# Kernel optimization log

Measured on AMD Instinct MI355X. Metric: run time of the kernel, lower is better.

Reference implementation:

```python
import jax, jax.numpy as jnp
import numpy as np

EYE_PENALTY = 1.0e6


def setup_inputs() -> dict:
    key = jax.random.key(0)
    k1, k2 = jax.random.split(key)
    B, NIN, NK, DK = 512, 1024, 128, 5
    x = jax.random.normal(k1, (B, NIN), dtype=jnp.float32)
    theta = jax.random.normal(k2, (NIN, NK, DK), dtype=jnp.float32) * 0.05
    log_weight_scale = jnp.zeros((NK, DK), dtype=jnp.float32)
    bias = jnp.full((NK,), -1.0, dtype=jnp.float32)
    return {"x": x, "theta": theta, "log_weight_scale": log_weight_scale, "bias": bias}


def reference(x, theta, log_weight_scale, bias):
    # kernel = theta * exp(log_weight_scale) / ||theta||_2 (norm over input dim)
    l2 = jnp.sqrt(jnp.sum(theta * theta, axis=0))            # [K, D]
    kernel = theta * (jnp.exp(log_weight_scale) / l2)[None]   # [NIN, K, D]
    actv = jnp.einsum('bi,ikd->bkd', x, kernel)               # [B, K, D]
    B = x.shape[0]
    # all-pairs L1 distance per kernel: [B, K, B]
    diff = actv[:, :, :, None] - jnp.transpose(actv, (1, 2, 0))[None]  # [B,K,D,B]
    abs_dif = jnp.sum(jnp.abs(diff), axis=2)                  # [B, K, B]
    abs_dif = abs_dif + EYE_PENALTY * jnp.eye(B, dtype=x.dtype)[:, None, :]
    f = jnp.sum(jnp.exp(-abs_dif), axis=2) + bias[None, :]    # [B, K]
    return jnp.concatenate([x, f], axis=1)                    # [B, NIN + K]
```

## Files before the change

### kernel.cpp

```cpp
#include <hip/hip_runtime.h>
#include <hip/hip_fp16.h>
#include <math.h>

constexpr int B    = 512;
constexpr int NIN  = 1024;
constexpr int NK   = 128;
constexpr int DK   = 5;
constexpr int NF   = NK * DK;
constexpr int NOUT = NIN + NK;
constexpr int SPLITK = 4;
constexpr int LDA = 88;
#define LOG2E 1.44269504088896f

typedef _Float16 f16x2 __attribute__((ext_vector_type(2)));
typedef _Float16 f16x4 __attribute__((ext_vector_type(4)));
typedef _Float16 f16x8 __attribute__((ext_vector_type(8)));
typedef float    f32x4 __attribute__((ext_vector_type(4)));

union H2 { __half2 h; f16x2 v; unsigned u; };

__global__ __launch_bounds__(256) void gemm_kernel(
        const float* __restrict__ x,
        const float* __restrict__ theta,
        float* __restrict__ actvP,
        float* __restrict__ ps) {
    __shared__ _Float16 Ath[64 * LDA];
    __shared__ _Float16 Bxh[64 * LDA];
    __shared__ float    red2[16][64];

    const int t    = threadIdx.x;
    const int tile = blockIdx.x >> 2;
    const int z    = blockIdx.x & 3;
    const int n0   = (tile >> 3) * 64;
    const int b0   = (tile & 7) * 64;
    const bool do_ps = (tile & 7) == 0;

    const int w   = t >> 6;
    const int l   = t & 63;
    const int r16 = l & 15;
    const int kg  = l >> 4;
    const int tk4 = t >> 4;
    const int tn4 = (t & 15) * 4;

    f32x4 acc0 = {0.f,0.f,0.f,0.f}, acc1 = {0.f,0.f,0.f,0.f};
    f32x4 acc2 = {0.f,0.f,0.f,0.f}, acc3 = {0.f,0.f,0.f,0.f};
    float sq0 = 0.f, sq1 = 0.f, sq2 = 0.f, sq3 = 0.f;

    for (int step = 0; step < 4; ++step) {
        const int kw = z * 256 + step * 64;
        const float4 v0 = *(const float4*)&theta[(kw + tk4*4 + 0)*NF + n0 + tn4];
        const float4 v1 = *(const float4*)&theta[(kw + tk4*4 + 1)*NF + n0 + tn4];
        const float4 v2 = *(const float4*)&theta[(kw + tk4*4 + 2)*NF + n0 + tn4];
        const float4 v3 = *(const float4*)&theta[(kw + tk4*4 + 3)*NF + n0 + tn4];
        if (do_ps) {
            sq0 += v0.x*v0.x + v1.x*v1.x + v2.x*v2.x + v3.x*v3.x;
            sq1 += v0.y*v0.y + v1.y*v1.y + v2.y*v2.y + v3.y*v3.y;
            sq2 += v0.z*v0.z + v1.z*v1.z + v2.z*v2.z + v3.z*v3.z;
            sq3 += v0.w*v0.w + v1.w*v1.w + v2.w*v2.w + v3.w*v3.w;
        }
        {
            f16x4 h;
            h[0]=(_Float16)v0.x; h[1]=(_Float16)v1.x; h[2]=(_Float16)v2.x; h[3]=(_Float16)v3.x;
            *(f16x4*)&Ath[(tn4+0)*LDA + tk4*4] = h;
            h[0]=(_Float16)v0.y; h[1]=(_Float16)v1.y; h[2]=(_Float16)v2.y; h[3]=(_Float16)v3.y;
            *(f16x4*)&Ath[(tn4+1)*LDA + tk4*4] = h;
            h[0]=(_Float16)v0.z; h[1]=(_Float16)v1.z; h[2]=(_Float16)v2.z; h[3]=(_Float16)v3.z;
            *(f16x4*)&Ath[(tn4+2)*LDA + tk4*4] = h;
            h[0]=(_Float16)v0.w; h[1]=(_Float16)v1.w; h[2]=(_Float16)v2.w; h[3]=(_Float16)v3.w;
            *(f16x4*)&Ath[(tn4+3)*LDA + tk4*4] = h;
        }
        #pragma unroll
        for (int i = 0; i < 4; ++i) {
            const int row = i * 16 + tk4;
            const float4 xv = *(const float4*)&x[(b0 + row)*NIN + kw + tn4];
            f16x4 h;
            h[0]=(_Float16)xv.x; h[1]=(_Float16)xv.y;
            h[2]=(_Float16)xv.z; h[3]=(_Float16)xv.w;
            *(f16x4*)&Bxh[row*LDA + tn4] = h;
        }
        __syncthreads();
        #pragma unroll
        for (int half = 0; half < 2; ++half) {
            const f16x8 av  = *(const f16x8*)&Ath[(w*16 + r16)*LDA + kg*8 + half*32];
            const f16x8 bv0 = *(const f16x8*)&Bxh[( 0 + r16)*LDA + kg*8 + half*32];
            const f16x8 bv1 = *(const f16x8*)&Bxh[(16 + r16)*LDA + kg*8 + half*32];
            const f16x8 bv2 = *(const f16x8*)&Bxh[(32 + r16)*LDA + kg*8 + half*32];
            const f16x8 bv3 = *(const f16x8*)&Bxh[(48 + r16)*LDA + kg*8 + half*32];
            acc0 = __builtin_amdgcn_mfma_f32_16x16x32_f16(av, bv0, acc0, 0, 0, 0);
            acc1 = __builtin_amdgcn_mfma_f32_16x16x32_f16(av, bv1, acc1, 0, 0, 0);
            acc2 = __builtin_amdgcn_mfma_f32_16x16x32_f16(av, bv2, acc2, 0, 0, 0);
            acc3 = __builtin_amdgcn_mfma_f32_16x16x32_f16(av, bv3, acc3, 0, 0, 0);
        }
        __syncthreads();
    }
    {
        float* dst = actvP + (size_t)z * NF * B
                   + (size_t)(n0 + w*16 + kg*4) * B + b0 + r16;
        #pragma unroll
        for (int j = 0; j < 4; ++j) {
            dst[j*B +  0] = acc0[j];
            dst[j*B + 16] = acc1[j];
            dst[j*B + 32] = acc2[j];
            dst[j*B + 48] = acc3[j];
        }
    }
    if (do_ps) {
        red2[tk4][tn4+0] = sq0; red2[tk4][tn4+1] = sq1;
        red2[tk4][tn4+2] = sq2; red2[tk4][tn4+3] = sq3;
        __syncthreads();
        if (t < 64) {
            float tot = 0.f;
            #pragma unroll
            for (int rr = 0; rr < 16; ++rr) tot += red2[rr][t];
            ps[z * NF + n0 + t] = tot;
        }
    }
}

__global__ __launch_bounds__(256) void rs_kernel(
        const float* __restrict__ actvP,
        const float* __restrict__ ps,
        const float* __restrict__ lws,
        __half* __restrict__ actv16) {
    const int t   = threadIdx.x;
    const int row = blockIdx.x * 2 + (t >> 7);
    const int c4  = (t & 127) * 4;

    const float nrm = ps[0*NF + row] + ps[1*NF + row]
                    + ps[2*NF + row] + ps[3*NF + row];
    const float s = __expf(lws[row]) * rsqrtf(nrm) * LOG2E;

    const float* p = actvP + (size_t)row * B + c4;
    float4 v0 = *(const float4*)(p + 0ull * NF * B);
    float4 v1 = *(const float4*)(p + 1ull * NF * B);
    float4 v2 = *(const float4*)(p + 2ull * NF * B);
    float4 v3 = *(const float4*)(p + 3ull * NF * B);
    f16x4 h;
    h[0] = (_Float16)((v0.x + v1.x + v2.x + v3.x) * s);
    h[1] = (_Float16)((v0.y + v1.y + v2.y + v3.y) * s);
    h[2] = (_Float16)((v0.z + v1.z + v2.z + v3.z) * s);
    h[3] = (_Float16)((v0.w + v1.w + v2.w + v3.w) * s);
    *(f16x4*)&actv16[(size_t)row * B + c4] = h;
}

__global__ __launch_bounds__(256) void pairwise_kernel(
        const __half* __restrict__ actv16,
        const float* __restrict__ bias,
        const float* __restrict__ x,
        float* __restrict__ out) {
    __shared__ __half a16s[DK * B];
    __shared__ float  red[8 * 64];

    const int k = blockIdx.x;
    const int e = blockIdx.y;
    const int t = threadIdx.x;

    if (e < 4) {
        const int row = k * 4 + e;
        ((float4*)out)[row * (NOUT/4) + t] = ((const float4*)x)[row * (NIN/4) + t];
    }

    {
        const uint4* src = (const uint4*)(actv16 + (size_t)k * DK * B);
        ((uint4*)a16s)[t] = src[t];
        if (t < 64) ((uint4*)a16s)[256 + t] = src[256 + t];
    }
    __syncthreads();

    const int g  = t >> 5;
    const int r  = t & 31;
    const int ba = e * 64 + r;
    const int bb = ba + 32;

    __half2 A2[DK], B2[DK];
    #pragma unroll
    for (int d = 0; d < DK; ++d) {
        A2[d] = __half2half2(a16s[d * B + ba]);
        B2[d] = __half2half2(a16s[d * B + bb]);
    }
    const H2 ones = {__half2half2(__float2half(1.0f))};

    float accA = 0.f, accB = 0.f;
    const int bp0 = g * 64;

    union W8 { f16x8 v; __half2 h[4]; };
    #pragma unroll 2
    for (int m = 0; m < 8; ++m) {
        const int bp = bp0 + m * 8;
        W8 w0, w1, w2, w3, w4;
        w0.v = *(const f16x8*)&a16s[0*B + bp];
        w1.v = *(const f16x8*)&a16s[1*B + bp];
        w2.v = *(const f16x8*)&a16s[2*B + bp];
        w3.v = *(const f16x8*)&a16s[3*B + bp];
        w4.v = *(const f16x8*)&a16s[4*B + bp];
        #pragma unroll
        for (int c = 0; c < 4; ++c) {
            __half2 dA = __habs2(__hsub2(A2[0], w0.h[c]));
            dA = __hadd2(dA, __habs2(__hsub2(A2[1], w1.h[c])));
            dA = __hadd2(dA, __habs2(__hsub2(A2[2], w2.h[c])));
            dA = __hadd2(dA, __habs2(__hsub2(A2[3], w3.h[c])));
            dA = __hadd2(dA, __habs2(__hsub2(A2[4], w4.h[c])));
            H2 eA; eA.h = h2exp2(__hneg2(dA));
            __half2 dB = __habs2(__hsub2(B2[0], w0.h[c]));
            dB = __hadd2(dB, __habs2(__hsub2(B2[1], w1.h[c])));
            dB = __hadd2(dB, __habs2(__hsub2(B2[2], w2.h[c])));
            dB = __hadd2(dB, __habs2(__hsub2(B2[3], w3.h[c])));
            dB = __hadd2(dB, __habs2(__hsub2(B2[4], w4.h[c])));
            H2 eB; eB.h = h2exp2(__hneg2(dB));
#if __has_builtin(__builtin_amdgcn_fdot2)
            accA = __builtin_amdgcn_fdot2(eA.v, ones.v, accA, false);
            accB = __builtin_amdgcn_fdot2(eB.v, ones.v, accB, false);
#else
            accA += __low2float(eA.h) + __high2float(eA.h);
            accB += __low2float(eB.h) + __high2float(eB.h);
#endif
        }
    }
    red[g * 64 + r]      = accA;
    red[g * 64 + 32 + r] = accB;
    __syncthreads();
    if (t < 64) {
        float f = -1.0f + bias[k];
        #pragma unroll
        for (int gg = 0; gg < 8; ++gg) f += red[gg * 64 + t];
        out[(e * 64 + t) * NOUT + NIN + k] = f;
    }
}

extern "C" void kernel_launch(void* const* d_in, const int* in_sizes, int n_in,
                              void* d_out, int out_size, void* d_ws, size_t ws_size,
                              hipStream_t stream) {
    const float* x     = (const float*)d_in[0];
    const float* theta = (const float*)d_in[1];
    const float* lws   = (const float*)d_in[2];
    const float* bias  = (const float*)d_in[3];
    float* out = (float*)d_out;

    char* wsb = (char*)d_ws;
    float*  ps     = (float*)wsb;
    float*  actvP  = (float*)(wsb + (64 << 10));
    __half* actv16 = (__half*)(wsb + (64 << 10) + 4 * sizeof(float) * NF * B);

    gemm_kernel<<<dim3(320), 256, 0, stream>>>(x, theta, actvP, ps);
    rs_kernel<<<dim3(320), 256, 0, stream>>>(actvP, ps, lws, actv16);
    pairwise_kernel<<<dim3(NK, 8), 256, 0, stream>>>(actv16, bias, x, out);
}
```

Before: 27.11 us.

## Raise GEMM split-K to 8 and load each K-chunk in a single pass

Doubles the split-K factor so the GEMM launches 640 blocks, each handling a 128-wide K slice loaded entirely into LDS at once. This removes the inner step loop and its per-step barriers, and issues all global loads up front for more memory-level parallelism. In exchange the split-K partial buffer doubles, so the reduction kernel reads twice as many partials. Register and LDS use per block also grow.

```diff
diff --git a/kernel.cpp b/kernel.cpp
--- a/kernel.cpp
+++ b/kernel.cpp
@@ -8,8 +8,8 @@
 constexpr int DK   = 5;
 constexpr int NF   = NK * DK;
 constexpr int NOUT = NIN + NK;
-constexpr int SPLITK = 4;
-constexpr int LDA = 88;
+constexpr int SPLITK = 8;
+constexpr int LDA = 136;
 #define LOG2E 1.44269504088896f
 
 typedef _Float16 f16x2 __attribute__((ext_vector_type(2)));
@@ -29,70 +29,82 @@
     __shared__ float    red2[16][64];
 
     const int t    = threadIdx.x;
-    const int tile = blockIdx.x >> 2;
-    const int z    = blockIdx.x & 3;
+    const int tile = blockIdx.x >> 3;
+    const int z    = blockIdx.x & 7;
     const int n0   = (tile >> 3) * 64;
     const int b0   = (tile & 7) * 64;
     const bool do_ps = (tile & 7) == 0;
+    const int kw   = z * 128;
+
+    const int kq  = t >> 4;
+    const int tn4 = (t & 15) * 4;
+    float4 tv[8];
+    #pragma unroll
+    for (int i = 0; i < 8; ++i)
+        tv[i] = *(const float4*)&theta[(kw + kq * 8 + i) * NF + n0 + tn4];
+
+    const int br = t >> 2;
+    const int ki = t & 3;
+    float4 xv[8];
+    #pragma unroll
+    for (int i = 0; i < 8; ++i)
+        xv[i] = *(const float4*)&x[(b0 + br) * NIN + kw + (ki + i * 4) * 4];
+
+    if (do_ps) {
+        float sq0 = 0.f, sq1 = 0.f, sq2 = 0.f, sq3 = 0.f;
+        #pragma unroll
+        for (int i = 0; i < 8; ++i) {
+            sq0 += tv[i].x * tv[i].x;  sq1 += tv[i].y * tv[i].y;
+            sq2 += tv[i].z * tv[i].z;  sq3 += tv[i].w * tv[i].w;
+        }
+        red2[kq][tn4 + 0] = sq0;  red2[kq][tn4 + 1] = sq1;
+        red2[kq][tn4 + 2] = sq2;  red2[kq][tn4 + 3] = sq3;
+    }
+
+    {
+        f16x8 h;
+        #pragma unroll
+        for (int i = 0; i < 8; ++i) h[i] = (_Float16)tv[i].x;
+        *(f16x8*)&Ath[(tn4 + 0) * LDA + kq * 8] = h;
+        #pragma unroll
+        for (int i = 0; i < 8; ++i) h[i] = (_Float16)tv[i].y;
+        *(f16x8*)&Ath[(tn4 + 1) * LDA + kq * 8] = h;
+        #pragma unroll
+        for (int i = 0; i < 8; ++i) h[i] = (_Float16)tv[i].z;
+        *(f16x8*)&Ath[(tn4 + 2) * LDA + kq * 8] = h;
+        #pragma unroll
+        for (int i = 0; i < 8; ++i) h[i] = (_Float16)tv[i].w;
+        *(f16x8*)&Ath[(tn4 + 3) * LDA + kq * 8] = h;
+    }
+    #pragma unroll
+    for (int i = 0; i < 8; ++i) {
+        f16x4 h;
+        h[0] = (_Float16)xv[i].x;  h[1] = (_Float16)xv[i].y;
+        h[2] = (_Float16)xv[i].z;  h[3] = (_Float16)xv[i].w;
+        *(f16x4*)&Bxh[br * LDA + (ki + i * 4) * 4] = h;
+    }
+    __syncthreads();
 
     const int w   = t >> 6;
     const int l   = t & 63;
     const int r16 = l & 15;
     const int kg  = l >> 4;
-    const int tk4 = t >> 4;
-    const int tn4 = (t & 15) * 4;
 
     f32x4 acc0 = {0.f,0.f,0.f,0.f}, acc1 = {0.f,0.f,0.f,0.f};
     f32x4 acc2 = {0.f,0.f,0.f,0.f}, acc3 = {0.f,0.f,0.f,0.f};
-    float sq0 = 0.f, sq1 = 0.f, sq2 = 0.f, sq3 = 0.f;
-
-    for (int step = 0; step < 4; ++step) {
-        const int kw = z * 256 + step * 64;
-        const float4 v0 = *(const float4*)&theta[(kw + tk4*4 + 0)*NF + n0 + tn4];
-        const float4 v1 = *(const float4*)&theta[(kw + tk4*4 + 1)*NF + n0 + tn4];
-        const float4 v2 = *(const float4*)&theta[(kw + tk4*4 + 2)*NF + n0 + tn4];
-        const float4 v3 = *(const float4*)&theta[(kw + tk4*4 + 3)*NF + n0 + tn4];
-        if (do_ps) {
-            sq0 += v0.x*v0.x + v1.x*v1.x + v2.x*v2.x + v3.x*v3.x;
-            sq1 += v0.y*v0.y + v1.y*v1.y + v2.y*v2.y + v3.y*v3.y;
-            sq2 += v0.z*v0.z + v1.z*v1.z + v2.z*v2.z + v3.z*v3.z;
-            sq3 += v0.w*v0.w + v1.w*v1.w + v2.w*v2.w + v3.w*v3.w;
-        }
-        {
-            f16x4 h;
-            h[0]=(_Float16)v0.x; h[1]=(_Float16)v1.x; h[2]=(_Float16)v2.x; h[3]=(_Float16)v3.x;
-            *(f16x4*)&Ath[(tn4+0)*LDA + tk4*4] = h;
-            h[0]=(_Float16)v0.y; h[1]=(_Float16)v1.y; h[2]=(_Float16)v2.y; h[3]=(_Float16)v3.y;
-            *(f16x4*)&Ath[(tn4+1)*LDA + tk4*4] = h;
-            h[0]=(_Float16)v0.z; h[1]=(_Float16)v1.z; h[2]=(_Float16)v2.z; h[3]=(_Float16)v3.z;
-            *(f16x4*)&Ath[(tn4+2)*LDA + tk4*4] = h;
-            h[0]=(_Float16)v0.w; h[1]=(_Float16)v1.w; h[2]=(_Float16)v2.w; h[3]=(_Float16)v3.w;
-            *(f16x4*)&Ath[(tn4+3)*LDA + tk4*4] = h;
-        }
-        #pragma unroll
-        for (int i = 0; i < 4; ++i) {
-            const int row = i * 16 + tk4;
-            const float4 xv = *(const float4*)&x[(b0 + row)*NIN + kw + tn4];
-            f16x4 h;
-            h[0]=(_Float16)xv.x; h[1]=(_Float16)xv.y;
-            h[2]=(_Float16)xv.z; h[3]=(_Float16)xv.w;
-            *(f16x4*)&Bxh[row*LDA + tn4] = h;
-        }
-        __syncthreads();
-        #pragma unroll
-        for (int half = 0; half < 2; ++half) {
-            const f16x8 av  = *(const f16x8*)&Ath[(w*16 + r16)*LDA + kg*8 + half*32];
-            const f16x8 bv0 = *(const f16x8*)&Bxh[( 0 + r16)*LDA + kg*8 + half*32];
-            const f16x8 bv1 = *(const f16x8*)&Bxh[(16 + r16)*LDA + kg*8 + half*32];
-            const f16x8 bv2 = *(const f16x8*)&Bxh[(32 + r16)*LDA + kg*8 + half*32];
-            const f16x8 bv3 = *(const f16x8*)&Bxh[(48 + r16)*LDA + kg*8 + half*32];
-            acc0 = __builtin_amdgcn_mfma_f32_16x16x32_f16(av, bv0, acc0, 0, 0, 0);
-            acc1 = __builtin_amdgcn_mfma_f32_16x16x32_f16(av, bv1, acc1, 0, 0, 0);
-            acc2 = __builtin_amdgcn_mfma_f32_16x16x32_f16(av, bv2, acc2, 0, 0, 0);
-            acc3 = __builtin_amdgcn_mfma_f32_16x16x32_f16(av, bv3, acc3, 0, 0, 0);
-        }
-        __syncthreads();
-    }
+    #pragma unroll
+    for (int ks = 0; ks < 4; ++ks) {
+        const f16x8 av  = *(const f16x8*)&Ath[(w*16 + r16)*LDA + ks*32 + kg*8];
+        const f16x8 bv0 = *(const f16x8*)&Bxh[( 0 + r16)*LDA + ks*32 + kg*8];
+        const f16x8 bv1 = *(const f16x8*)&Bxh[(16 + r16)*LDA + ks*32 + kg*8];
+        const f16x8 bv2 = *(const f16x8*)&Bxh[(32 + r16)*LDA + ks*32 + kg*8];
+        const f16x8 bv3 = *(const f16x8*)&Bxh[(48 + r16)*LDA + ks*32 + kg*8];
+        acc0 = __builtin_amdgcn_mfma_f32_16x16x32_f16(av, bv0, acc0, 0, 0, 0);
+        acc1 = __builtin_amdgcn_mfma_f32_16x16x32_f16(av, bv1, acc1, 0, 0, 0);
+        acc2 = __builtin_amdgcn_mfma_f32_16x16x32_f16(av, bv2, acc2, 0, 0, 0);
+        acc3 = __builtin_amdgcn_mfma_f32_16x16x32_f16(av, bv3, acc3, 0, 0, 0);
+    }
+
     {
         float* dst = actvP + (size_t)z * NF * B
                    + (size_t)(n0 + w*16 + kg*4) * B + b0 + r16;
@@ -105,8 +117,6 @@
         }
     }
     if (do_ps) {
-        red2[tk4][tn4+0] = sq0; red2[tk4][tn4+1] = sq1;
-        red2[tk4][tn4+2] = sq2; red2[tk4][tn4+3] = sq3;
         __syncthreads();
         if (t < 64) {
             float tot = 0.f;
@@ -126,20 +136,23 @@
     const int row = blockIdx.x * 2 + (t >> 7);
     const int c4  = (t & 127) * 4;
 
-    const float nrm = ps[0*NF + row] + ps[1*NF + row]
-                    + ps[2*NF + row] + ps[3*NF + row];
+    float nrm = 0.f;
+    #pragma unroll
+    for (int zz = 0; zz < SPLITK; ++zz) nrm += ps[zz * NF + row];
     const float s = __expf(lws[row]) * rsqrtf(nrm) * LOG2E;
 
     const float* p = actvP + (size_t)row * B + c4;
-    float4 v0 = *(const float4*)(p + 0ull * NF * B);
-    float4 v1 = *(const float4*)(p + 1ull * NF * B);
-    float4 v2 = *(const float4*)(p + 2ull * NF * B);
-    float4 v3 = *(const float4*)(p + 3ull * NF * B);
+    float4 vs = *(const float4*)(p);
+    #pragma unroll
+    for (int zz = 1; zz < SPLITK; ++zz) {
+        const float4 v = *(const float4*)(p + (size_t)zz * NF * B);
+        vs.x += v.x; vs.y += v.y; vs.z += v.z; vs.w += v.w;
+    }
     f16x4 h;
-    h[0] = (_Float16)((v0.x + v1.x + v2.x + v3.x) * s);
-    h[1] = (_Float16)((v0.y + v1.y + v2.y + v3.y) * s);
-    h[2] = (_Float16)((v0.z + v1.z + v2.z + v3.z) * s);
-    h[3] = (_Float16)((v0.w + v1.w + v2.w + v3.w) * s);
+    h[0] = (_Float16)(vs.x * s);
+    h[1] = (_Float16)(vs.y * s);
+    h[2] = (_Float16)(vs.z * s);
+    h[3] = (_Float16)(vs.w * s);
     *(f16x4*)&actv16[(size_t)row * B + c4] = h;
 }
 
@@ -239,9 +252,10 @@
     char* wsb = (char*)d_ws;
     float*  ps     = (float*)wsb;
     float*  actvP  = (float*)(wsb + (64 << 10));
-    __half* actv16 = (__half*)(wsb + (64 << 10) + 4 * sizeof(float) * NF * B);
-
-    gemm_kernel<<<dim3(320), 256, 0, stream>>>(x, theta, actvP, ps);
+    __half* actv16 = (__half*)(wsb + (64 << 10)
+                               + (size_t)SPLITK * sizeof(float) * NF * B);
+
+    gemm_kernel<<<dim3(640), 256, 0, stream>>>(x, theta, actvP, ps);
     rs_kernel<<<dim3(320), 256, 0, stream>>>(actvP, ps, lws, actv16);
     pairwise_kernel<<<dim3(NK, 8), 256, 0, stream>>>(actv16, bias, x, out);
 }
```

Result: slower. 28.44 us (+4.9%).
